# Kernel optimization log

Hardware: AMD Instinct MI355X
Metric: run time of the kernel (lower is better)

## Reference

```python
import jax, jax.numpy as jnp
import numpy as np

N, E, F, EF, D, G = 25000, 100000, 32, 8, 64, 1000


def setup_inputs() -> dict:
    key = jax.random.key(0)
    ks = jax.random.split(key, 32)
    p = lambda k, shape: (jax.random.normal(k, shape, jnp.float32) * 0.05)
    inp = {
        "x": jax.random.normal(ks[0], (N, F), jnp.float32),
        "edge_index": jax.random.randint(ks[1], (2, E), 0, N, jnp.int64 if jax.config.jax_enable_x64 else jnp.int32),
        "edge_attr": jax.random.uniform(ks[2], (E, EF), jnp.float32),
        "batch": jnp.sort(jax.random.randint(ks[3], (N,), 0, G, jnp.int32)),
        # lin0
        "W0": p(ks[4], (F, D)), "b0": p(ks[5], (D,)),
        # edge MLP: Linear(EF, D) -> ReLU -> Linear(D, D*D)
        "We1": p(ks[6], (EF, D)), "be1": p(ks[7], (D,)),
        "We2": p(ks[8], (D, D * D)), "be2": p(ks[9], (D * D,)),
        # NNConv root weight + bias
        "Wroot": p(ks[10], (D, D)), "bconv": p(ks[11], (D,)),
        # GRU (single layer): gate order r, z, n
        "Wi": p(ks[12], (3 * D, D)), "Wh": p(ks[13], (3 * D, D)),
        "bi": p(ks[14], (3 * D,)), "bh": p(ks[15], (3 * D,)),
        # heads
        "W11": p(ks[16], (D, D)), "b11": p(ks[17], (D,)),
        "W12": p(ks[18], (D, D)), "b12": p(ks[19], (D,)),
        "W13": p(ks[20], (D, 1)), "b13": p(ks[21], (1,)),
        "W21": p(ks[22], (D, D)), "b21": p(ks[23], (D,)),
        "W22": p(ks[24], (D, D)), "b22": p(ks[25], (D,)),
        "W23": p(ks[26], (D, 1)), "b23": p(ks[27], (1,)),
    }
    return inp


def reference(x, edge_index, edge_attr, batch,
              W0, b0, We1, be1, We2, be2, Wroot, bconv,
              Wi, Wh, bi, bh,
              W11, b11, W12, b12, W13, b13,
              W21, b21, W22, b22, W23, b23):
    src, dst = edge_index[0], edge_index[1]
    # lin0 + relu
    x1 = jax.nn.relu(x @ W0 + b0)                      # [N, D]
    h = x1                                              # GRU hidden init
    # NNConv: dynamic per-edge weight via edge MLP
    ew = (jax.nn.relu(edge_attr @ We1 + be1) @ We2 + be2).reshape(E, D, D)
    msg = jnp.einsum('ei,eio->eo', x1[src], ew)        # per-edge matmul
    agg = jax.ops.segment_sum(msg, dst, num_segments=N)
    x2 = jax.nn.relu(x1 @ Wroot + agg + bconv)         # [N, D]
    # GRU single step (torch gate order: r, z, n)
    gi = x2 @ Wi.T + bi
    gh = h @ Wh.T + bh
    r = jax.nn.sigmoid(gi[:, :D] + gh[:, :D])
    z = jax.nn.sigmoid(gi[:, D:2 * D] + gh[:, D:2 * D])
    n = jnp.tanh(gi[:, 2 * D:] + r * gh[:, 2 * D:])
    hn = (1.0 - z) * n + z * h                          # [N, D]
    # graph pooling (scatter_add over batch)
    pooled = jax.ops.segment_sum(hn, batch, num_segments=G)  # [G, D]
    # two MLP heads
    x_1 = jax.nn.relu(pooled @ W11 + b11)
    x_1 = jax.nn.relu(x_1 @ W12 + b12)
    x_1 = x_1 @ W13 + b13
    x_2 = jax.nn.relu(pooled @ W21 + b21)
    x_2 = jax.nn.relu(x_2 @ W22 + b22)
    x_2 = x_2 @ W23 + b23
    return jnp.concatenate([x_1, x_2], axis=1)          # [G, 2]
```

## Files before the change

### kernel.cpp

```cpp
#include <hip/hip_runtime.h>
#include <hip/hip_bf16.h>

#define NN 25000
#define NE 100000
#define FIN 32
#define DD 64
#define NG 1000

typedef unsigned short u16;
typedef __attribute__((ext_vector_type(8))) short short8;
typedef __attribute__((ext_vector_type(4))) float f32x4;

__device__ __forceinline__ float b2f(u16 u) {
    union { unsigned int i; float f; } v; v.i = ((unsigned int)u) << 16; return v.f;
}
__device__ __forceinline__ u16 f2b(float f) {
    __hip_bfloat16 h = __float2bfloat16(f);
    return __builtin_bit_cast(u16, h);
}
__device__ __forceinline__ bool idx_is_i64(const int* e) {
    return (e[1] == 0) & (e[3] == 0) & (e[5] == 0) & (e[7] == 0) & (e[9] == 0);
}
__device__ __forceinline__ int ld_src(const int* e, int i, bool i64) {
    return i64 ? e[2 * i] : e[i];
}
__device__ __forceinline__ int ld_dst(const int* e, int i, bool i64) {
    return i64 ? e[2 * (NE + i)] : e[NE + i];
}

__global__ __launch_bounds__(256) void k_pre(const float* __restrict__ x,
                                             const float* __restrict__ W0,
                                             const float* __restrict__ b0,
                                             u16* __restrict__ x1b,
                                             const float* __restrict__ We2,
                                             const float* __restrict__ be2,
                                             float* __restrict__ agg,
                                             float* __restrict__ pooled,
                                             u16* __restrict__ Bt2) {
    __shared__ float sW[FIN * DD];
    __shared__ float sx[4 * FIN];
    if (blockIdx.x < 6250) {
        int tid = threadIdx.x;
        for (int i = tid; i < FIN * DD; i += 256) sW[i] = W0[i];
        int nbase = blockIdx.x * 4;
        for (int i = tid; i < 4 * FIN; i += 256) {
            int nl = i >> 5, f = i & 31;
            int n = nbase + nl;
            sx[i] = (n < NN) ? x[n * FIN + f] : 0.f;
        }
        __syncthreads();
        int lane = tid & 63, nl = tid >> 6;
        int n = nbase + nl;
        if (n < NN) {
            float acc = b0[lane];
            #pragma unroll
            for (int f = 0; f < FIN; f++) acc += sx[nl * FIN + f] * sW[f * DD + lane];
            x1b[n * DD + lane] = f2b(fmaxf(acc, 0.f));
        }
    } else {
        int tid = (blockIdx.x - 6250) * 256 + threadIdx.x;
        int stride = 1024 * 256;
        for (int idx = tid; idx < 65 * 4096; idx += stride) {
            int kc = idx >> 12;
            int rem = idx & 4095;
            int f = rem >> 9;
            int ln = (rem >> 3) & 63;
            int j = idx & 7;
            int s = f >> 2, c = f & 3;
            int o = c * 16 + (ln & 15);
            int r = kc * 64 + s * 32 + (ln >> 4) * 8 + j;
            float v = (r < 4096) ? We2[(r >> 6) * 4096 + (r & 63) * 64 + o]
                                 : be2[(r - 4096) * 64 + o];
            Bt2[idx] = f2b(v);
        }
        for (int idx = tid; idx < NN * DD; idx += stride) agg[idx] = 0.f;
        for (int idx = tid; idx < NG * DD; idx += stride) pooled[idx] = 0.f;
    }
}

__global__ __launch_bounds__(256) void k_msg(const float* __restrict__ ea,
                                             const int* __restrict__ eidx,
                                             const float* __restrict__ We1,
                                             const float* __restrict__ be1,
                                             const u16* __restrict__ x1b,
                                             const u16* __restrict__ Bt2,
                                             float* __restrict__ agg) {
    __shared__ __align__(16) u16 sX[128 * 72];
    __shared__ u16 sT[64 * 128];
    __shared__ float sWe1[8 * 64];
    __shared__ float sbe1[64];
    __shared__ int sDst[128];
    const int tid = threadIdx.x;
    const int lane = tid & 63, wv = tid >> 6;
    const int ll = lane & 15, quad = lane >> 4;
    const int e0 = blockIdx.x * 128;
    const bool i64 = idx_is_i64(eidx);

    for (int i = tid; i < 512; i += 256) sWe1[i] = We1[i];
    if (tid < 64) sbe1[tid] = be1[tid];
    if (tid < 128) sDst[tid] = (e0 + tid < NE) ? ld_dst(eidx, e0 + tid, i64) : 0;

    const int eg2 = e0 + (tid >> 1);
    {
        int i0 = (tid & 1) * 32;
        if (eg2 < NE) {
            int sv = ld_src(eidx, eg2, i64);
            const u16* xr = x1b + sv * 64 + i0;
            #pragma unroll
            for (int c = 0; c < 4; c++)
                *(uint4*)&sX[(tid >> 1) * 72 + i0 + c * 8] = *(const uint4*)(xr + c * 8);
        } else {
            uint4 z = make_uint4(0, 0, 0, 0);
            #pragma unroll
            for (int c = 0; c < 4; c++)
                *(uint4*)&sX[(tid >> 1) * 72 + i0 + c * 8] = z;
        }
    }
    float eav[8];
    if (eg2 < NE) {
        f32x4 v0 = *(const f32x4*)(ea + eg2 * 8);
        f32x4 v1 = *(const f32x4*)(ea + eg2 * 8 + 4);
        #pragma unroll
        for (int f = 0; f < 4; f++) { eav[f] = v0[f]; eav[4 + f] = v1[f]; }
    } else {
        #pragma unroll
        for (int f = 0; f < 8; f++) eav[f] = 0.f;
    }
    __syncthreads();

    {
        int e = tid >> 1, k0 = (tid & 1) * 32;
        for (int kk = 0; kk < 32; kk++) {
            int k = k0 + kk;
            float acc = sbe1[k];
            #pragma unroll
            for (int f = 0; f < 8; f++) acc += eav[f] * sWe1[f * 64 + k];
            sT[k * 128 + e] = (eg2 < NE) ? f2b(fmaxf(acc, 0.f)) : (u16)0;
        }
    }
    __syncthreads();

    short8 xa[8][2];
    #pragma unroll
    for (int rt = 0; rt < 8; rt++)
        #pragma unroll
        for (int s = 0; s < 2; s++)
            xa[rt][s] = *(const short8*)&sX[(rt * 16 + ll) * 72 + s * 32 + quad * 8];

    f32x4 msg[8];
    #pragma unroll
    for (int rt = 0; rt < 8; rt++) msg[rt] = (f32x4){0.f, 0.f, 0.f, 0.f};

    const u16* gB0 = Bt2 + (0 * 4 + wv) * 512 + lane * 8;
    const u16* gB1 = Bt2 + (1 * 4 + wv) * 512 + lane * 8;

    short8 bf0 = *(const short8*)gB0;
    short8 bf1 = *(const short8*)gB1;
    const f32x4 zero = (f32x4){0.f, 0.f, 0.f, 0.f};

    for (int kc = 0; kc <= 64; kc++) {
        int knxt = (kc < 64) ? (kc + 1) : 64;
        short8 bn0 = *(const short8*)(gB0 + knxt * 4096);
        short8 bn1 = *(const short8*)(gB1 + knxt * 4096);

        float tk[8][4];
        if (kc < 64) {
            #pragma unroll
            for (int rt = 0; rt < 8; rt++) {
                const u16* tp = &sT[kc * 128 + rt * 16 + quad * 4];
                #pragma unroll
                for (int r = 0; r < 4; r++) tk[rt][r] = b2f(tp[r]);
            }
        } else {
            #pragma unroll
            for (int rt = 0; rt < 8; rt++)
                #pragma unroll
                for (int r = 0; r < 4; r++) tk[rt][r] = 1.f;
        }

        #pragma unroll
        for (int rt = 0; rt < 8; rt++) {
            f32x4 q = __builtin_amdgcn_mfma_f32_16x16x32_bf16(xa[rt][0], bf0, zero, 0, 0, 0);
            q = __builtin_amdgcn_mfma_f32_16x16x32_bf16(xa[rt][1], bf1, q, 0, 0, 0);
            #pragma unroll
            for (int r = 0; r < 4; r++) msg[rt][r] += tk[rt][r] * q[r];
        }
        bf0 = bn0; bf1 = bn1;
    }

    #pragma unroll
    for (int rt = 0; rt < 8; rt++) {
        #pragma unroll
        for (int r = 0; r < 4; r++) {
            int el = rt * 16 + quad * 4 + r;
            int eg = e0 + el;
            if (eg < NE) {
                int d = sDst[el];
                atomicAdd(&agg[d * 64 + wv * 16 + ll], msg[rt][r]);
            }
        }
    }
}

__global__ __launch_bounds__(256) void k_gru(const u16* __restrict__ x1b,
                                             const float* __restrict__ agg,
                                             const float* __restrict__ Wroot,
                                             const float* __restrict__ bconv,
                                             const float* __restrict__ Wi,
                                             const float* __restrict__ Wh,
                                             const float* __restrict__ bi,
                                             const float* __restrict__ bh,
                                             const int* __restrict__ batch,
                                             float* __restrict__ pooled) {
    __shared__ __align__(16) u16 sWi[192 * 72];
    __shared__ __align__(16) u16 sWh[192 * 72];
    __shared__ __align__(16) u16 sX2[64 * 72];
    __shared__ int sBatch[64];
    const int tid = threadIdx.x;
    const int lane = tid & 63, wv = tid >> 6;
    const int ll = lane & 15, quad = lane >> 4;
    const int n0 = blockIdx.x * 64;

    for (int idx = tid; idx < 4096; idx += 256) {
        int n = idx >> 6, k = idx & 63;
        sWi[n * 72 + k] = f2b(Wroot[k * 64 + n]);
    }
    if (tid < 64) {
        int n = n0 + tid;
        sBatch[tid] = (n < NN) ? batch[n] : -1;
    }
    __syncthreads();

    short8 ha[2];
    {
        int n = n0 + wv * 16 + ll;
        #pragma unroll
        for (int kc = 0; kc < 2; kc++) {
            if (n < NN) ha[kc] = *(const short8*)(x1b + n * 64 + kc * 32 + quad * 8);
            else        ha[kc] = (short8){0,0,0,0,0,0,0,0};
        }
    }
    f32x4 acc1[4];
    #pragma unroll
    for (int c = 0; c < 4; c++) acc1[c] = (f32x4){0.f, 0.f, 0.f, 0.f};
    #pragma unroll
    for (int kc = 0; kc < 2; kc++) {
        #pragma unroll
        for (int c = 0; c < 4; c++) {
            short8 b = *(const short8*)&sWi[(c * 16 + ll) * 72 + kc * 32 + quad * 8];
            acc1[c] = __builtin_amdgcn_mfma_f32_16x16x32_bf16(ha[kc], b, acc1[c], 0, 0, 0);
        }
    }
    #pragma unroll
    for (int c = 0; c < 4; c++) {
        int col = c * 16 + ll;
        float bcv = bconv[col];
        #pragma unroll
        for (int r = 0; r < 4; r++) {
            int row = wv * 16 + quad * 4 + r;
            int n = n0 + row;
            float v = 0.f;
            if (n < NN) v = fmaxf(acc1[c][r] + agg[n * 64 + col] + bcv, 0.f);
            sX2[row * 72 + col] = f2b(v);
        }
    }
    __syncthreads();

    for (int idx = tid; idx < 192 * 64; idx += 256) {
        int j = idx >> 6, i = idx & 63;
        sWi[j * 72 + i] = f2b(Wi[idx]);
        sWh[j * 72 + i] = f2b(Wh[idx]);
    }
    __syncthreads();

    short8 xa[2];
    #pragma unroll
    for (int kc = 0; kc < 2; kc++)
        xa[kc] = *(const short8*)&sX2[(wv * 16 + ll) * 72 + kc * 32 + quad * 8];

    f32x4 agi[12], agh[12];
    #pragma unroll
    for (int c = 0; c < 12; c++) { agi[c] = (f32x4){0.f,0.f,0.f,0.f}; agh[c] = (f32x4){0.f,0.f,0.f,0.f}; }
    #pragma unroll
    for (int kc = 0; kc < 2; kc++) {
        #pragma unroll
        for (int c = 0; c < 12; c++) {
            short8 bi8 = *(const short8*)&sWi[(c * 16 + ll) * 72 + kc * 32 + quad * 8];
            short8 bh8 = *(const short8*)&sWh[(c * 16 + ll) * 72 + kc * 32 + quad * 8];
            agi[c] = __builtin_amdgcn_mfma_f32_16x16x32_bf16(xa[kc], bi8, agi[c], 0, 0, 0);
            agh[c] = __builtin_amdgcn_mfma_f32_16x16x32_bf16(ha[kc], bh8, agh[c], 0, 0, 0);
        }
    }

    float hnv[4][4];
    #pragma unroll
    for (int c0 = 0; c0 < 4; c0++) {
        int d = c0 * 16 + ll;
        float bir = bi[d],        bhr = bh[d];
        float biz = bi[64 + d],   bhz = bh[64 + d];
        float bin = bi[128 + d],  bhn = bh[128 + d];
        #pragma unroll
        for (int r = 0; r < 4; r++) {
            int row = wv * 16 + quad * 4 + r;
            int n = n0 + row;
            float gir = agi[c0][r] + bir,     ghr = agh[c0][r] + bhr;
            float giz = agi[c0 + 4][r] + biz, ghz = agh[c0 + 4][r] + bhz;
            float gin = agi[c0 + 8][r] + bin, ghn = agh[c0 + 8][r] + bhn;
            float rg = 1.f / (1.f + __expf(-(gir + ghr)));
            float zg = 1.f / (1.f + __expf(-(giz + ghz)));
            float ng = tanhf(gin + rg * ghn);
            float hv = (n < NN) ? b2f(x1b[n * 64 + d]) : 0.f;
            hnv[c0][r] = (n < NN) ? ((1.f - zg) * ng + zg * hv) : 0.f;
        }
    }
    __syncthreads();

    float* hbuf = (float*)sWi;
    #pragma unroll
    for (int c0 = 0; c0 < 4; c0++) {
        int d = c0 * 16 + ll;
        #pragma unroll
        for (int r = 0; r < 4; r++) {
            int row = wv * 16 + quad * 4 + r;
            hbuf[row * 65 + d] = hnv[c0][r];
        }
    }
    __syncthreads();

    {
        int d = lane;
        float sum = 0.f;
        int pb = sBatch[wv * 16];
        #pragma unroll
        for (int rr = 0; rr < 16; rr++) {
            int row = wv * 16 + rr;
            int b = sBatch[row];
            float v = hbuf[row * 65 + d];
            if (b != pb) {
                if (pb >= 0) atomicAdd(&pooled[pb * 64 + d], sum);
                sum = v; pb = b;
            } else {
                sum += v;
            }
        }
        if (pb >= 0) atomicAdd(&pooled[pb * 64 + d], sum);
    }
}

__global__ __launch_bounds__(256) void k_heads(const float* __restrict__ pooled,
                                               const float* __restrict__ W11, const float* __restrict__ b11,
                                               const float* __restrict__ W12, const float* __restrict__ b12,
                                               const float* __restrict__ W13, const float* __restrict__ b13,
                                               const float* __restrict__ W21, const float* __restrict__ b21,
                                               const float* __restrict__ W22, const float* __restrict__ b22,
                                               const float* __restrict__ W23, const float* __restrict__ b23,
                                               float* __restrict__ out) {
    __shared__ float sV[4][64];
    __shared__ float sA[4][64];
    int tid = threadIdx.x, lane = tid & 63, wv = tid >> 6;
    int g = blockIdx.x * 4 + wv;
    if (g >= NG) return;
    float p = pooled[g * 64 + lane];
    sV[wv][lane] = p;
    float y[2];
    const float* W1s[2] = {W11, W21}; const float* b1s[2] = {b11, b21};
    const float* W2s[2] = {W12, W22}; const float* b2s[2] = {b12, b22};
    const float* W3s[2] = {W13, W23}; const float* b3s[2] = {b13, b23};
    #pragma unroll
    for (int hd = 0; hd < 2; hd++) {
        float a = b1s[hd][lane];
        #pragma unroll 8
        for (int i = 0; i < 64; i++) a += sV[wv][i] * W1s[hd][i * 64 + lane];
        a = fmaxf(a, 0.f);
        sA[wv][lane] = a;
        float a2 = b2s[hd][lane];
        #pragma unroll 8
        for (int i = 0; i < 64; i++) a2 += sA[wv][i] * W2s[hd][i * 64 + lane];
        a2 = fmaxf(a2, 0.f);
        float part = a2 * W3s[hd][lane];
        #pragma unroll
        for (int m = 32; m > 0; m >>= 1) part += __shfl_xor(part, m, 64);
        y[hd] = part + b3s[hd][0];
    }
    if (lane == 0) {
        out[g * 2 + 0] = y[0];
        out[g * 2 + 1] = y[1];
    }
}

extern "C" void kernel_launch(void* const* d_in, const int* in_sizes, int n_in,
                              void* d_out, int out_size, void* d_ws, size_t ws_size,
                              hipStream_t stream) {
    const float* x     = (const float*)d_in[0];
    const int* eidx    = (const int*)d_in[1];
    const float* ea    = (const float*)d_in[2];
    const int* batch   = (const int*)d_in[3];
    const float* W0    = (const float*)d_in[4];  const float* b0    = (const float*)d_in[5];
    const float* We1   = (const float*)d_in[6];  const float* be1   = (const float*)d_in[7];
    const float* We2   = (const float*)d_in[8];  const float* be2   = (const float*)d_in[9];
    const float* Wroot = (const float*)d_in[10]; const float* bconv = (const float*)d_in[11];
    const float* Wi    = (const float*)d_in[12]; const float* Wh    = (const float*)d_in[13];
    const float* bi    = (const float*)d_in[14]; const float* bh    = (const float*)d_in[15];
    const float* W11   = (const float*)d_in[16]; const float* b11   = (const float*)d_in[17];
    const float* W12   = (const float*)d_in[18]; const float* b12   = (const float*)d_in[19];
    const float* W13   = (const float*)d_in[20]; const float* b13   = (const float*)d_in[21];
    const float* W21   = (const float*)d_in[22]; const float* b21   = (const float*)d_in[23];
    const float* W22   = (const float*)d_in[24]; const float* b22   = (const float*)d_in[25];
    const float* W23   = (const float*)d_in[26]; const float* b23   = (const float*)d_in[27];
    float* out = (float*)d_out;

    char* ws = (char*)d_ws;
    float* agg    = (float*)(ws);
    u16*   x1b    = (u16*)(ws + 6400000);
    u16*   Bt2    = (u16*)(ws + 9600000);
    float* pooled = (float*)(ws + 10132480);

    hipLaunchKernelGGL(k_pre, dim3(7274), dim3(256), 0, stream,
                       x, W0, b0, x1b, We2, be2, agg, pooled, Bt2);
    hipLaunchKernelGGL(k_msg, dim3(782), dim3(256), 0, stream, ea, eidx, We1, be1, x1b, Bt2, agg);
    hipLaunchKernelGGL(k_gru, dim3(391), dim3(256), 0, stream, x1b, agg, Wroot, bconv,
                       Wi, Wh, bi, bh, batch, pooled);
    hipLaunchKernelGGL(k_heads, dim3(250), dim3(256), 0, stream, pooled,
                       W11, b11, W12, b12, W13, b13, W21, b21, W22, b22, W23, b23, out);
}
```

Baseline: 258.4 us.

## Restructure edge-message MMA to stage edge weights in LDS and scale A operand

The per-edge message kernel now stages chunks of the precomputed second-layer weight tiles (Bt2) into shared memory in groups of four k-chunks. Each wave owns 32 edges and all 64 output columns, rather than 16 columns across all 128 edges. The hidden activation is folded into the A operand (t_k * x, rounded to bf16) so MFMAs accumulate directly, replacing the separate FMA scaling of each partial product. The GRU kernel's weight loads into LDS are vectorized into 4-wide stores. The cost is extra barriers, extra bf16 rounding of the scaled inputs, and more atomics per thread.

```diff
diff --git a/kernel.cpp b/kernel.cpp
--- a/kernel.cpp
+++ b/kernel.cpp
@@ -85,7 +85,7 @@
                                              const u16* __restrict__ x1b,
                                              const u16* __restrict__ Bt2,
                                              float* __restrict__ agg) {
-    __shared__ __align__(16) u16 sX[128 * 72];
+    __shared__ __align__(16) u16 sB[16384];
     __shared__ u16 sT[64 * 128];
     __shared__ float sWe1[8 * 64];
     __shared__ float sbe1[64];
@@ -95,6 +95,7 @@
     const int ll = lane & 15, quad = lane >> 4;
     const int e0 = blockIdx.x * 128;
     const bool i64 = idx_is_i64(eidx);
+    u16* sX = sB;
 
     for (int i = tid; i < 512; i += 256) sWe1[i] = We1[i];
     if (tid < 64) sbe1[tid] = be1[tid];
@@ -140,63 +141,84 @@
     }
     __syncthreads();
 
-    short8 xa[8][2];
-    #pragma unroll
-    for (int rt = 0; rt < 8; rt++)
-        #pragma unroll
-        for (int s = 0; s < 2; s++)
-            xa[rt][s] = *(const short8*)&sX[(rt * 16 + ll) * 72 + s * 32 + quad * 8];
-
-    f32x4 msg[8];
-    #pragma unroll
-    for (int rt = 0; rt < 8; rt++) msg[rt] = (f32x4){0.f, 0.f, 0.f, 0.f};
-
-    const u16* gB0 = Bt2 + (0 * 4 + wv) * 512 + lane * 8;
-    const u16* gB1 = Bt2 + (1 * 4 + wv) * 512 + lane * 8;
-
-    short8 bf0 = *(const short8*)gB0;
-    short8 bf1 = *(const short8*)gB1;
-    const f32x4 zero = (f32x4){0.f, 0.f, 0.f, 0.f};
-
-    for (int kc = 0; kc <= 64; kc++) {
-        int knxt = (kc < 64) ? (kc + 1) : 64;
-        short8 bn0 = *(const short8*)(gB0 + knxt * 4096);
-        short8 bn1 = *(const short8*)(gB1 + knxt * 4096);
-
-        float tk[8][4];
-        if (kc < 64) {
-            #pragma unroll
-            for (int rt = 0; rt < 8; rt++) {
-                const u16* tp = &sT[kc * 128 + rt * 16 + quad * 4];
+    float xsf[2][2][8];
+    short8 xab[2][2];
+    #pragma unroll
+    for (int rt = 0; rt < 2; rt++)
+        #pragma unroll
+        for (int s = 0; s < 2; s++) {
+            short8 v = *(const short8*)&sX[(wv * 32 + rt * 16 + ll) * 72 + s * 32 + quad * 8];
+            xab[rt][s] = v;
+            #pragma unroll
+            for (int j = 0; j < 8; j++) xsf[rt][s][j] = b2f((u16)v[j]);
+        }
+
+    f32x4 acc[2][4];
+    #pragma unroll
+    for (int rt = 0; rt < 2; rt++)
+        #pragma unroll
+        for (int c = 0; c < 4; c++) acc[rt][c] = (f32x4){0.f, 0.f, 0.f, 0.f};
+
+    for (int g = 0; g < 17; g++) {
+        const int nch = (g < 16) ? 4 : 1;
+        __syncthreads();
+        for (int r = 0; r < nch * 2; r++) {
+            int o = r * 2048 + tid * 8;
+            *(uint4*)&sB[o] = *(const uint4*)&Bt2[g * 16384 + o];
+        }
+        __syncthreads();
+
+        for (int ch = 0; ch < nch; ch++) {
+            const int kc = g * 4 + ch;
+            const u16* bbase = sB + ch * 4096;
+            short8 bfr[2][4];
+            #pragma unroll
+            for (int s = 0; s < 2; s++)
                 #pragma unroll
-                for (int r = 0; r < 4; r++) tk[rt][r] = b2f(tp[r]);
+                for (int c = 0; c < 4; c++)
+                    bfr[s][c] = *(const short8*)(bbase + (s * 4 + c) * 512 + lane * 8);
+
+            if (kc < 64) {
+                float tk0 = b2f(sT[kc * 128 + wv * 32 + ll]);
+                float tk1 = b2f(sT[kc * 128 + wv * 32 + 16 + ll]);
+                #pragma unroll
+                for (int s = 0; s < 2; s++) {
+                    short8 a0, a1;
+                    #pragma unroll
+                    for (int j = 0; j < 8; j++) {
+                        a0[j] = (short)f2b(tk0 * xsf[0][s][j]);
+                        a1[j] = (short)f2b(tk1 * xsf[1][s][j]);
+                    }
+                    #pragma unroll
+                    for (int c = 0; c < 4; c++) {
+                        acc[0][c] = __builtin_amdgcn_mfma_f32_16x16x32_bf16(a0, bfr[s][c], acc[0][c], 0, 0, 0);
+                        acc[1][c] = __builtin_amdgcn_mfma_f32_16x16x32_bf16(a1, bfr[s][c], acc[1][c], 0, 0, 0);
+                    }
+                }
+            } else {
+                #pragma unroll
+                for (int s = 0; s < 2; s++)
+                    #pragma unroll
+                    for (int c = 0; c < 4; c++) {
+                        acc[0][c] = __builtin_amdgcn_mfma_f32_16x16x32_bf16(xab[0][s], bfr[s][c], acc[0][c], 0, 0, 0);
+                        acc[1][c] = __builtin_amdgcn_mfma_f32_16x16x32_bf16(xab[1][s], bfr[s][c], acc[1][c], 0, 0, 0);
+                    }
             }
-        } else {
-            #pragma unroll
-            for (int rt = 0; rt < 8; rt++)
-                #pragma unroll
-                for (int r = 0; r < 4; r++) tk[rt][r] = 1.f;
-        }
-
-        #pragma unroll
-        for (int rt = 0; rt < 8; rt++) {
-            f32x4 q = __builtin_amdgcn_mfma_f32_16x16x32_bf16(xa[rt][0], bf0, zero, 0, 0, 0);
-            q = __builtin_amdgcn_mfma_f32_16x16x32_bf16(xa[rt][1], bf1, q, 0, 0, 0);
-            #pragma unroll
-            for (int r = 0; r < 4; r++) msg[rt][r] += tk[rt][r] * q[r];
-        }
-        bf0 = bn0; bf1 = bn1;
-    }
-
-    #pragma unroll
-    for (int rt = 0; rt < 8; rt++) {
+        }
+    }
+
+    #pragma unroll
+    for (int rt = 0; rt < 2; rt++) {
+        int elb = wv * 32 + rt * 16 + quad * 4;
         #pragma unroll
         for (int r = 0; r < 4; r++) {
-            int el = rt * 16 + quad * 4 + r;
+            int el = elb + r;
             int eg = e0 + el;
             if (eg < NE) {
                 int d = sDst[el];
-                atomicAdd(&agg[d * 64 + wv * 16 + ll], msg[rt][r]);
+                #pragma unroll
+                for (int c = 0; c < 4; c++)
+                    atomicAdd(&agg[d * 64 + c * 16 + ll], acc[rt][c][r]);
             }
         }
     }
@@ -221,9 +243,14 @@
     const int ll = lane & 15, quad = lane >> 4;
     const int n0 = blockIdx.x * 64;
 
-    for (int idx = tid; idx < 4096; idx += 256) {
-        int n = idx >> 6, k = idx & 63;
-        sWi[n * 72 + k] = f2b(Wroot[k * 64 + n]);
+    for (int idx = tid; idx < 64 * 16; idx += 256) {
+        int n = idx & 63, k4 = (idx >> 6) * 4;
+        ushort4 a;
+        a.x = f2b(Wroot[(k4 + 0) * 64 + n]);
+        a.y = f2b(Wroot[(k4 + 1) * 64 + n]);
+        a.z = f2b(Wroot[(k4 + 2) * 64 + n]);
+        a.w = f2b(Wroot[(k4 + 3) * 64 + n]);
+        *(ushort4*)&sWi[n * 72 + k4] = a;
     }
     if (tid < 64) {
         int n = n0 + tid;
@@ -266,10 +293,15 @@
     }
     __syncthreads();
 
-    for (int idx = tid; idx < 192 * 64; idx += 256) {
-        int j = idx >> 6, i = idx & 63;
-        sWi[j * 72 + i] = f2b(Wi[idx]);
-        sWh[j * 72 + i] = f2b(Wh[idx]);
+    for (int idx = tid; idx < 192 * 16; idx += 256) {
+        int j = idx >> 4, i4 = (idx & 15) * 4;
+        float4 wi4 = *(const float4*)&Wi[j * 64 + i4];
+        float4 wh4 = *(const float4*)&Wh[j * 64 + i4];
+        ushort4 a, b;
+        a.x = f2b(wi4.x); a.y = f2b(wi4.y); a.z = f2b(wi4.z); a.w = f2b(wi4.w);
+        b.x = f2b(wh4.x); b.y = f2b(wh4.y); b.z = f2b(wh4.z); b.w = f2b(wh4.w);
+        *(ushort4*)&sWi[j * 72 + i4] = a;
+        *(ushort4*)&sWh[j * 72 + i4] = b;
     }
     __syncthreads();
 
```

Result: slower. 271.4 us (+5.0%).

## Split k_msg edge tile across 8 waves and vectorize GRU weight staging

Applied to the files above, without the earlier changes.

The message kernel now runs 512 threads per block. Each wave handles half of the 128 edges (4 row tiles instead of 8) for one 16-column output quarter, and the bias step is peeled out of the main loop. This cuts per-wave register pressure and serial MFMA work, at the cost of each B fragment being loaded from global memory by twice as many waves. The GRU kernel's weight staging into shared memory now uses vectorized float4 loads and ushort4 stores instead of scalar ones.

```diff
diff --git a/kernel.cpp b/kernel.cpp
--- a/kernel.cpp
+++ b/kernel.cpp
@@ -78,13 +78,13 @@
     }
 }
 
-__global__ __launch_bounds__(256) void k_msg(const float* __restrict__ ea,
-                                             const int* __restrict__ eidx,
-                                             const float* __restrict__ We1,
-                                             const float* __restrict__ be1,
-                                             const u16* __restrict__ x1b,
-                                             const u16* __restrict__ Bt2,
-                                             float* __restrict__ agg) {
+__global__ __launch_bounds__(512, 4) void k_msg(const float* __restrict__ ea,
+                                                const int* __restrict__ eidx,
+                                                const float* __restrict__ We1,
+                                                const float* __restrict__ be1,
+                                                const u16* __restrict__ x1b,
+                                                const u16* __restrict__ Bt2,
+                                                float* __restrict__ agg) {
     __shared__ __align__(16) u16 sX[128 * 72];
     __shared__ u16 sT[64 * 128];
     __shared__ float sWe1[8 * 64];
@@ -93,33 +93,32 @@
     const int tid = threadIdx.x;
     const int lane = tid & 63, wv = tid >> 6;
     const int ll = lane & 15, quad = lane >> 4;
+    const int rh = wv >> 2, cq = wv & 3;
     const int e0 = blockIdx.x * 128;
     const bool i64 = idx_is_i64(eidx);
 
-    for (int i = tid; i < 512; i += 256) sWe1[i] = We1[i];
+    if (tid < 512) sWe1[tid] = We1[tid];
     if (tid < 64) sbe1[tid] = be1[tid];
     if (tid < 128) sDst[tid] = (e0 + tid < NE) ? ld_dst(eidx, e0 + tid, i64) : 0;
 
-    const int eg2 = e0 + (tid >> 1);
+    const int el4 = tid >> 2, seg = tid & 3;
+    const int eg4 = e0 + el4;
     {
-        int i0 = (tid & 1) * 32;
-        if (eg2 < NE) {
-            int sv = ld_src(eidx, eg2, i64);
-            const u16* xr = x1b + sv * 64 + i0;
-            #pragma unroll
-            for (int c = 0; c < 4; c++)
-                *(uint4*)&sX[(tid >> 1) * 72 + i0 + c * 8] = *(const uint4*)(xr + c * 8);
+        if (eg4 < NE) {
+            int sv = ld_src(eidx, eg4, i64);
+            const u16* xr = x1b + sv * 64 + seg * 16;
+            *(uint4*)&sX[el4 * 72 + seg * 16]     = *(const uint4*)(xr);
+            *(uint4*)&sX[el4 * 72 + seg * 16 + 8] = *(const uint4*)(xr + 8);
         } else {
             uint4 z = make_uint4(0, 0, 0, 0);
-            #pragma unroll
-            for (int c = 0; c < 4; c++)
-                *(uint4*)&sX[(tid >> 1) * 72 + i0 + c * 8] = z;
+            *(uint4*)&sX[el4 * 72 + seg * 16]     = z;
+            *(uint4*)&sX[el4 * 72 + seg * 16 + 8] = z;
         }
     }
     float eav[8];
-    if (eg2 < NE) {
-        f32x4 v0 = *(const f32x4*)(ea + eg2 * 8);
-        f32x4 v1 = *(const f32x4*)(ea + eg2 * 8 + 4);
+    if (eg4 < NE) {
+        f32x4 v0 = *(const f32x4*)(ea + eg4 * 8);
+        f32x4 v1 = *(const f32x4*)(ea + eg4 * 8 + 4);
         #pragma unroll
         for (int f = 0; f < 4; f++) { eav[f] = v0[f]; eav[4 + f] = v1[f]; }
     } else {
@@ -129,57 +128,49 @@
     __syncthreads();
 
     {
-        int e = tid >> 1, k0 = (tid & 1) * 32;
-        for (int kk = 0; kk < 32; kk++) {
+        int k0 = seg * 16;
+        for (int kk = 0; kk < 16; kk++) {
             int k = k0 + kk;
             float acc = sbe1[k];
             #pragma unroll
             for (int f = 0; f < 8; f++) acc += eav[f] * sWe1[f * 64 + k];
-            sT[k * 128 + e] = (eg2 < NE) ? f2b(fmaxf(acc, 0.f)) : (u16)0;
-        }
-    }
-    __syncthreads();
-
-    short8 xa[8][2];
-    #pragma unroll
-    for (int rt = 0; rt < 8; rt++)
+            sT[k * 128 + el4] = (eg4 < NE) ? f2b(fmaxf(acc, 0.f)) : (u16)0;
+        }
+    }
+    __syncthreads();
+
+    short8 xa[4][2];
+    #pragma unroll
+    for (int rt = 0; rt < 4; rt++)
         #pragma unroll
         for (int s = 0; s < 2; s++)
-            xa[rt][s] = *(const short8*)&sX[(rt * 16 + ll) * 72 + s * 32 + quad * 8];
-
-    f32x4 msg[8];
-    #pragma unroll
-    for (int rt = 0; rt < 8; rt++) msg[rt] = (f32x4){0.f, 0.f, 0.f, 0.f};
-
-    const u16* gB0 = Bt2 + (0 * 4 + wv) * 512 + lane * 8;
-    const u16* gB1 = Bt2 + (1 * 4 + wv) * 512 + lane * 8;
+            xa[rt][s] = *(const short8*)&sX[(rh * 64 + rt * 16 + ll) * 72 + s * 32 + quad * 8];
+
+    f32x4 msg[4];
+    #pragma unroll
+    for (int rt = 0; rt < 4; rt++) msg[rt] = (f32x4){0.f, 0.f, 0.f, 0.f};
+
+    const u16* gB0 = Bt2 + (0 * 4 + cq) * 512 + lane * 8;
+    const u16* gB1 = Bt2 + (1 * 4 + cq) * 512 + lane * 8;
 
     short8 bf0 = *(const short8*)gB0;
     short8 bf1 = *(const short8*)gB1;
     const f32x4 zero = (f32x4){0.f, 0.f, 0.f, 0.f};
 
-    for (int kc = 0; kc <= 64; kc++) {
-        int knxt = (kc < 64) ? (kc + 1) : 64;
-        short8 bn0 = *(const short8*)(gB0 + knxt * 4096);
-        short8 bn1 = *(const short8*)(gB1 + knxt * 4096);
-
-        float tk[8][4];
-        if (kc < 64) {
+    for (int kc = 0; kc < 64; kc++) {
+        short8 bn0 = *(const short8*)(gB0 + (kc + 1) * 4096);
+        short8 bn1 = *(const short8*)(gB1 + (kc + 1) * 4096);
+
+        float tk[4][4];
+        #pragma unroll
+        for (int rt = 0; rt < 4; rt++) {
+            const u16* tp = &sT[kc * 128 + rh * 64 + rt * 16 + quad * 4];
             #pragma unroll
-            for (int rt = 0; rt < 8; rt++) {
-                const u16* tp = &sT[kc * 128 + rt * 16 + quad * 4];
-                #pragma unroll
-                for (int r = 0; r < 4; r++) tk[rt][r] = b2f(tp[r]);
-            }
-        } else {
-            #pragma unroll
-            for (int rt = 0; rt < 8; rt++)
-                #pragma unroll
-                for (int r = 0; r < 4; r++) tk[rt][r] = 1.f;
-        }
-
-        #pragma unroll
-        for (int rt = 0; rt < 8; rt++) {
+            for (int r = 0; r < 4; r++) tk[rt][r] = b2f(tp[r]);
+        }
+
+        #pragma unroll
+        for (int rt = 0; rt < 4; rt++) {
             f32x4 q = __builtin_amdgcn_mfma_f32_16x16x32_bf16(xa[rt][0], bf0, zero, 0, 0, 0);
             q = __builtin_amdgcn_mfma_f32_16x16x32_bf16(xa[rt][1], bf1, q, 0, 0, 0);
             #pragma unroll
@@ -187,16 +178,23 @@
         }
         bf0 = bn0; bf1 = bn1;
     }
-
-    #pragma unroll
-    for (int rt = 0; rt < 8; rt++) {
+    #pragma unroll
+    for (int rt = 0; rt < 4; rt++) {
+        f32x4 q = __builtin_amdgcn_mfma_f32_16x16x32_bf16(xa[rt][0], bf0, zero, 0, 0, 0);
+        q = __builtin_amdgcn_mfma_f32_16x16x32_bf16(xa[rt][1], bf1, q, 0, 0, 0);
+        #pragma unroll
+        for (int r = 0; r < 4; r++) msg[rt][r] += q[r];
+    }
+
+    #pragma unroll
+    for (int rt = 0; rt < 4; rt++) {
         #pragma unroll
         for (int r = 0; r < 4; r++) {
-            int el = rt * 16 + quad * 4 + r;
+            int el = rh * 64 + rt * 16 + quad * 4 + r;
             int eg = e0 + el;
             if (eg < NE) {
                 int d = sDst[el];
-                atomicAdd(&agg[d * 64 + wv * 16 + ll], msg[rt][r]);
+                atomicAdd(&agg[d * 64 + cq * 16 + ll], msg[rt][r]);
             }
         }
     }
@@ -221,9 +219,14 @@
     const int ll = lane & 15, quad = lane >> 4;
     const int n0 = blockIdx.x * 64;
 
-    for (int idx = tid; idx < 4096; idx += 256) {
-        int n = idx >> 6, k = idx & 63;
-        sWi[n * 72 + k] = f2b(Wroot[k * 64 + n]);
+    for (int idx = tid; idx < 64 * 16; idx += 256) {
+        int n = idx & 63, k4 = (idx >> 6) * 4;
+        ushort4 a;
+        a.x = f2b(Wroot[(k4 + 0) * 64 + n]);
+        a.y = f2b(Wroot[(k4 + 1) * 64 + n]);
+        a.z = f2b(Wroot[(k4 + 2) * 64 + n]);
+        a.w = f2b(Wroot[(k4 + 3) * 64 + n]);
+        *(ushort4*)&sWi[n * 72 + k4] = a;
     }
     if (tid < 64) {
         int n = n0 + tid;
@@ -266,10 +269,15 @@
     }
     __syncthreads();
 
-    for (int idx = tid; idx < 192 * 64; idx += 256) {
-        int j = idx >> 6, i = idx & 63;
-        sWi[j * 72 + i] = f2b(Wi[idx]);
-        sWh[j * 72 + i] = f2b(Wh[idx]);
+    for (int idx = tid; idx < 192 * 16; idx += 256) {
+        int j = idx >> 4, i4 = (idx & 15) * 4;
+        float4 wi4 = *(const float4*)&Wi[j * 64 + i4];
+        float4 wh4 = *(const float4*)&Wh[j * 64 + i4];
+        ushort4 a, b;
+        a.x = f2b(wi4.x); a.y = f2b(wi4.y); a.z = f2b(wi4.z); a.w = f2b(wi4.w);
+        b.x = f2b(wh4.x); b.y = f2b(wh4.y); b.z = f2b(wh4.z); b.w = f2b(wh4.w);
+        *(ushort4*)&sWi[j * 72 + i4] = a;
+        *(ushort4*)&sWh[j * 72 + i4] = b;
     }
     __syncthreads();
 
@@ -417,7 +425,7 @@
 
     hipLaunchKernelGGL(k_pre, dim3(7274), dim3(256), 0, stream,
                        x, W0, b0, x1b, We2, be2, agg, pooled, Bt2);
-    hipLaunchKernelGGL(k_msg, dim3(782), dim3(256), 0, stream, ea, eidx, We1, be1, x1b, Bt2, agg);
+    hipLaunchKernelGGL(k_msg, dim3(782), dim3(512), 0, stream, ea, eidx, We1, be1, x1b, Bt2, agg);
     hipLaunchKernelGGL(k_gru, dim3(391), dim3(256), 0, stream, x1b, agg, Wroot, bconv,
                        Wi, Wh, bi, bh, batch, pooled);
     hipLaunchKernelGGL(k_heads, dim3(250), dim3(256), 0, stream, pooled,
```

New measurement: 237.2 us. 1.09x faster.
